# Optimization experiments

Measured on AMD Instinct MI355X. Metric: run time of the kernel, lower is better.

The kernel has to match this reference:

```python
import jax, jax.numpy as jnp
import numpy as np

N, E, G = 50000, 600000, 256
D, L, V = 128, 5, 128
BN_EPS = 1e-5


def setup_inputs() -> dict:
    key = jax.random.key(0)
    ks = jax.random.split(key, 24)
    x = jax.random.randint(ks[0], (N, 9), 0, V)
    edge_index = jax.random.randint(ks[1], (2, E), 0, N)
    edge_attr = jax.random.randint(ks[2], (E, 3), 0, V)
    batch = jnp.sort(jax.random.randint(ks[3], (N,), 0, G))
    s = 0.02
    inp = dict(
        x=x, edge_index=edge_index, edge_attr=edge_attr, batch=batch,
        atom_emb=jax.random.normal(ks[4], (9, V, D)) * s,
        bond_emb=jax.random.normal(ks[5], (L, 3, V, D)) * s,
        eps=jnp.zeros((L,)),
        W1=jax.random.normal(ks[6], (D, 2 * D)) * s, b1=jnp.zeros((2 * D,)),
        g1=jnp.ones((2 * D,)), be1=jnp.zeros((2 * D,)),
        W2=jax.random.normal(ks[7], (2 * D, D)) * s, b2=jnp.zeros((D,)),
        bn_g=jnp.ones((L, D)), bn_b=jnp.zeros((L, D)),
        fcW1=jax.random.normal(ks[8], (D, 1024)) * s, fcb1=jnp.zeros((1024,)),
        fcW2=jax.random.normal(ks[9], (1024, 1024)) * s, fcb2=jnp.zeros((1024,)),
        fcW3=jax.random.normal(ks[10], (1024, 512)) * s, fcb3=jnp.zeros((512,)),
        fcW4=jax.random.normal(ks[11], (512, 1)) * s, fcb4=jnp.zeros((1,)),
    )
    return inp


def _bn(h, g, b):
    # training-mode batchnorm (biased variance, as torch uses for normalization)
    m = h.mean(0)
    v = jnp.var(h, axis=0)
    return (h - m) * jax.lax.rsqrt(v + BN_EPS) * g + b


def _embed(tables, idx):
    # tables: [F, V, D], idx: [M, F] -> sum over F of table lookups -> [M, D]
    F = tables.shape[0]
    return tables[jnp.arange(F)[None, :], idx].sum(axis=1)


def reference(x, edge_index, edge_attr, batch, atom_emb, bond_emb, eps,
              W1, b1, g1, be1, W2, b2, bn_g, bn_b,
              fcW1, fcb1, fcW2, fcb2, fcW3, fcb3, fcW4, fcb4):
    src, dst = edge_index[0], edge_index[1]

    def mlp(h):
        z = jax.nn.relu(_bn(h @ W1 + b1, g1, be1))
        return z @ W2 + b2

    h = _embed(atom_emb, x)  # AtomEncoder: [N, D]
    h_sum = h  # JK='sum' accumulator
    for l in range(L):
        e = _embed(bond_emb[l], edge_attr)            # BondEncoder: [E, D]
        msg = jax.nn.relu(h[src] + e)                  # gather + elementwise
        agg = jax.ops.segment_sum(msg, dst, num_segments=N)  # scatter-add
        h = mlp((1.0 + eps[l]) * h + agg)
        h = _bn(h, bn_g[l], bn_b[l])
        if l < L - 1:
            h = jax.nn.relu(h)
        # dropout is identity in eval mode
        h_sum = h_sum + h

    # global mean pool over graphs
    sums = jax.ops.segment_sum(h_sum, batch, num_segments=G)
    cnts = jax.ops.segment_sum(jnp.ones((N,), h_sum.dtype), batch, num_segments=G)
    rep = sums / jnp.maximum(cnts, 1.0)[:, None]

    z = jax.nn.relu(rep @ fcW1 + fcb1)
    z = jax.nn.relu(z @ fcW2 + fcb2)
    z = jax.nn.relu(z @ fcW3 + fcb3)
    out = (z @ fcW4 + fcb4).squeeze(-1)  # [G]
    return out
```

## Files before the change

### kernel.cpp

```cpp
#include <hip/hip_runtime.h>

typedef unsigned short u16;
typedef unsigned int u32;
typedef __bf16 bf16x8 __attribute__((ext_vector_type(8)));
typedef float f32x4 __attribute__((ext_vector_type(4)));

#define NN 50000
#define EE 600000
#define GG 256
#define LL 5
#define NB 196

__device__ __forceinline__ float b2f(u16 u) {
  unsigned int v = ((unsigned int)u) << 16;
  return __builtin_bit_cast(float, v);
}
__device__ __forceinline__ u16 f2b(float f) {
  unsigned int u = __builtin_bit_cast(unsigned int, f);
  u += 0x7FFFu + ((u >> 16) & 1u);
  return (u16)(u >> 16);
}

__global__ void k_detect(const u32* __restrict__ w, int* __restrict__ flag) {
  __shared__ int sh[256];
  u32 v = w[threadIdx.x];
  u32 lo = v & 0xFFFFu;
  u32 e = (lo >> 7) & 0xFFu;
  sh[threadIdx.x] = (e >= 0x60u && e <= 0x7Fu) ? 1 : 0;
  __syncthreads();
  for (int s = 128; s > 0; s >>= 1) {
    if (threadIdx.x < (unsigned)s) sh[threadIdx.x] += sh[threadIdx.x + s];
    __syncthreads();
  }
  if (threadIdx.x == 0) flag[0] = (sh[0] < 128) ? 1 : 0;
}

struct CvtArgs {
  const void* src[19];
  u16* dst[19];
  int cum[20];
};

__global__ void k_cvt_all(CvtArgs a, const int* __restrict__ flag) {
  int t = blockIdx.x * 256 + threadIdx.x;
  if (t >= a.cum[19]) return;
  int i = 0;
  while (t >= a.cum[i + 1]) ++i;
  int j = t - a.cum[i];
  if (flag[0]) a.dst[i][j] = f2b(((const float*)a.src[i])[j]);
  else a.dst[i][j] = ((const u16*)a.src[i])[j];
}

__global__ void k_tr(const u16* __restrict__ src, u16* __restrict__ dst, int K, int N) {
  __shared__ u16 t[32][33];
  const int kb = blockIdx.x * 32, nb = blockIdx.y * 32;
  const int tx = threadIdx.x & 31, ty = threadIdx.x >> 5;
#pragma unroll
  for (int i = ty; i < 32; i += 8) t[i][tx] = src[(kb + i) * N + nb + tx];
  __syncthreads();
#pragma unroll
  for (int i = ty; i < 32; i += 8) dst[(nb + i) * K + kb + tx] = t[tx][i];
}

__global__ void k_init(int* __restrict__ deg, float* __restrict__ rep,
                       float* __restrict__ bnbuf, int* __restrict__ gstart,
                       int* __restrict__ gend) {
  int i = blockIdx.x * 256 + threadIdx.x;
  if (i < NN) deg[i] = 0;
  if (i < GG * 128) rep[i] = 0.f;
  if (i < 768) bnbuf[i] = 0.f;
  if (i < GG) { gstart[i] = 0; gend[i] = -1; }
}

__global__ void k_deg(const int* __restrict__ ei, int* __restrict__ deg) {
  int e = blockIdx.x * 256 + threadIdx.x;
  if (e < EE) atomicAdd(&deg[ei[EE + e]], 1);
}

__global__ void k_scan1(const int* __restrict__ deg, int* __restrict__ rowp,
                        int* __restrict__ bsum) {
  __shared__ int sh[256];
  int i = blockIdx.x * 256 + threadIdx.x;
  int v = (i < NN) ? deg[i] : 0;
  sh[threadIdx.x] = v;
  __syncthreads();
  for (int s = 1; s < 256; s <<= 1) {
    int t = (threadIdx.x >= (unsigned)s) ? sh[threadIdx.x - s] : 0;
    __syncthreads();
    sh[threadIdx.x] += t;
    __syncthreads();
  }
  if (i < NN) rowp[i] = sh[threadIdx.x] - v;
  if (threadIdx.x == 255) bsum[blockIdx.x] = sh[255];
}

__global__ void k_scan2(int* __restrict__ bsum, int* __restrict__ boff) {
  __shared__ int sh[256];
  int v = (threadIdx.x < NB) ? bsum[threadIdx.x] : 0;
  sh[threadIdx.x] = v;
  __syncthreads();
  for (int s = 1; s < 256; s <<= 1) {
    int t = (threadIdx.x >= (unsigned)s) ? sh[threadIdx.x - s] : 0;
    __syncthreads();
    sh[threadIdx.x] += t;
    __syncthreads();
  }
  if (threadIdx.x < NB) boff[threadIdx.x] = sh[threadIdx.x] - v;
}

__global__ void k_scan3(int* __restrict__ rowp, const int* __restrict__ boff,
                        int* __restrict__ cursor) {
  int i = blockIdx.x * 256 + threadIdx.x;
  if (i < NN) {
    int r = rowp[i] + boff[blockIdx.x];
    rowp[i] = r;
    cursor[i] = r;
  }
  if (i == 0) rowp[NN] = EE;
}

__global__ void k_fill(const int* __restrict__ ei, const int* __restrict__ eattr,
                       int* __restrict__ cursor, uint2* __restrict__ epack) {
  int e = blockIdx.x * 256 + threadIdx.x;
  if (e < EE) {
    int d = ei[EE + e];
    int pos = atomicAdd(&cursor[d], 1);
    u32 src = (u32)ei[e];
    u32 a0 = (u32)eattr[e * 3], a1 = (u32)eattr[e * 3 + 1], a2 = (u32)eattr[e * 3 + 2];
    epack[pos] = make_uint2(src | (a0 << 16) | (a1 << 23), a2);
  }
}

__global__ void k_gb(const int* __restrict__ batch, int* __restrict__ gstart,
                     int* __restrict__ gend) {
  int n = blockIdx.x * 256 + threadIdx.x;
  if (n >= NN) return;
  int b = batch[n];
  if (n == 0 || batch[n - 1] != b) gstart[b] = n;
  if (n == NN - 1 || batch[n + 1] != b) gend[b] = n;
}

__global__ void k_atom(const int* __restrict__ x, const u16* __restrict__ aemb,
                       u16* __restrict__ h) {
  int idx = blockIdx.x * 256 + threadIdx.x;
  if (idx >= NN * 64) return;
  int n = idx >> 6, f2 = (idx & 63) << 1;
  float a0 = 0.f, a1 = 0.f;
#pragma unroll
  for (int j = 0; j < 9; ++j) {
    int xv = x[n * 9 + j];
    u32 v = *(const u32*)(aemb + (j * 128 + xv) * 128 + f2);
    a0 += b2f((u16)v);
    a1 += b2f((u16)(v >> 16));
  }
  u32 o = (u32)f2b(a0) | ((u32)f2b(a1) << 16);
  *(u32*)(h + n * 128 + f2) = o;
}

__global__ __launch_bounds__(256)
void k_pull(const u16* __restrict__ h, const int* __restrict__ rowp,
            const uint2* __restrict__ epack, const u16* __restrict__ bond,
            const u16* __restrict__ epsv, int layer, u16* __restrict__ amat) {
  const int lane = threadIdx.x & 63;
  const int node = blockIdx.x * 4 + (threadIdx.x >> 6);
  const int p0 = rowp[node], p1 = rowp[node + 1];
  const int lo = lane << 1;
  const u16* bondB = bond + 16384;
  const u16* bondC = bond + 32768;
  float acc0 = 0.f, acc1 = 0.f;
  int p = p0;
  for (; p + 4 <= p1; p += 4) {
    uint2 e0 = epack[p], e1 = epack[p + 1], e2 = epack[p + 2], e3 = epack[p + 3];
    u32 h0 = *(const u32*)(h + (size_t)(e0.x & 0xFFFFu) * 128 + lo);
    u32 h1 = *(const u32*)(h + (size_t)(e1.x & 0xFFFFu) * 128 + lo);
    u32 h2 = *(const u32*)(h + (size_t)(e2.x & 0xFFFFu) * 128 + lo);
    u32 h3 = *(const u32*)(h + (size_t)(e3.x & 0xFFFFu) * 128 + lo);
    u32 a0 = *(const u32*)(bond + ((e0.x >> 16) & 0x7Fu) * 128 + lo);
    u32 a1 = *(const u32*)(bond + ((e1.x >> 16) & 0x7Fu) * 128 + lo);
    u32 a2 = *(const u32*)(bond + ((e2.x >> 16) & 0x7Fu) * 128 + lo);
    u32 a3 = *(const u32*)(bond + ((e3.x >> 16) & 0x7Fu) * 128 + lo);
    u32 b0 = *(const u32*)(bondB + ((e0.x >> 23) & 0x7Fu) * 128 + lo);
    u32 b1 = *(const u32*)(bondB + ((e1.x >> 23) & 0x7Fu) * 128 + lo);
    u32 b2 = *(const u32*)(bondB + ((e2.x >> 23) & 0x7Fu) * 128 + lo);
    u32 b3 = *(const u32*)(bondB + ((e3.x >> 23) & 0x7Fu) * 128 + lo);
    u32 c0 = *(const u32*)(bondC + e0.y * 128 + lo);
    u32 c1 = *(const u32*)(bondC + e1.y * 128 + lo);
    u32 c2 = *(const u32*)(bondC + e2.y * 128 + lo);
    u32 c3 = *(const u32*)(bondC + e3.y * 128 + lo);
    acc0 += fmaxf(b2f((u16)h0) + b2f((u16)a0) + b2f((u16)b0) + b2f((u16)c0), 0.f);
    acc1 += fmaxf(b2f((u16)(h0 >> 16)) + b2f((u16)(a0 >> 16)) + b2f((u16)(b0 >> 16)) + b2f((u16)(c0 >> 16)), 0.f);
    acc0 += fmaxf(b2f((u16)h1) + b2f((u16)a1) + b2f((u16)b1) + b2f((u16)c1), 0.f);
    acc1 += fmaxf(b2f((u16)(h1 >> 16)) + b2f((u16)(a1 >> 16)) + b2f((u16)(b1 >> 16)) + b2f((u16)(c1 >> 16)), 0.f);
    acc0 += fmaxf(b2f((u16)h2) + b2f((u16)a2) + b2f((u16)b2) + b2f((u16)c2), 0.f);
    acc1 += fmaxf(b2f((u16)(h2 >> 16)) + b2f((u16)(a2 >> 16)) + b2f((u16)(b2 >> 16)) + b2f((u16)(c2 >> 16)), 0.f);
    acc0 += fmaxf(b2f((u16)h3) + b2f((u16)a3) + b2f((u16)b3) + b2f((u16)c3), 0.f);
    acc1 += fmaxf(b2f((u16)(h3 >> 16)) + b2f((u16)(a3 >> 16)) + b2f((u16)(b3 >> 16)) + b2f((u16)(c3 >> 16)), 0.f);
  }
  for (; p < p1; ++p) {
    uint2 e0 = epack[p];
    u32 h0 = *(const u32*)(h + (size_t)(e0.x & 0xFFFFu) * 128 + lo);
    u32 a0 = *(const u32*)(bond + ((e0.x >> 16) & 0x7Fu) * 128 + lo);
    u32 b0 = *(const u32*)(bondB + ((e0.x >> 23) & 0x7Fu) * 128 + lo);
    u32 c0 = *(const u32*)(bondC + e0.y * 128 + lo);
    acc0 += fmaxf(b2f((u16)h0) + b2f((u16)a0) + b2f((u16)b0) + b2f((u16)c0), 0.f);
    acc1 += fmaxf(b2f((u16)(h0 >> 16)) + b2f((u16)(a0 >> 16)) + b2f((u16)(b0 >> 16)) + b2f((u16)(c0 >> 16)), 0.f);
  }
  float epsf = 1.0f + b2f(epsv[layer]);
  u32 own = *(const u32*)(h + (size_t)node * 128 + lo);
  u32 o = (u32)f2b(epsf * b2f((u16)own) + acc0) |
          ((u32)f2b(epsf * b2f((u16)(own >> 16)) + acc1) << 16);
  *(u32*)(amat + (size_t)node * 128 + lo) = o;
}

__global__ __launch_bounds__(256, 2)
void k_gemm1(const u16* __restrict__ amat, const u16* __restrict__ w1t,
             const u16* __restrict__ b1, u16* __restrict__ z0,
             float* __restrict__ bnsum, float* __restrict__ bnsq) {
  __shared__ u16 As[128 * 72];
  __shared__ u16 Bs[128 * 72];
  __shared__ float colAcc[256];
  const int tid = threadIdx.x;
  const int r0 = blockIdx.x * 128;
  const int nc = blockIdx.y * 128;
  const int w = tid >> 6, lane = tid & 63, l15 = lane & 15, q = lane >> 4;
  const int wr = (w & 1) * 64, wc = (w >> 1) * 64;
  f32x4 acc[4][4];
#pragma unroll
  for (int i = 0; i < 4; ++i)
#pragma unroll
    for (int j = 0; j < 4; ++j) acc[i][j] = {0.f, 0.f, 0.f, 0.f};

#pragma unroll
  for (int ks = 0; ks < 2; ++ks) {
    const int k0 = ks * 64;
    for (int idx = tid; idx < 1024; idx += 256) {
      const int row = idx >> 3, c8 = (idx & 7) << 3;
      int gr = r0 + row; if (gr >= NN) gr = NN - 1;
      uint4 va = *(const uint4*)(amat + (size_t)gr * 128 + k0 + c8);
      *(uint4*)(As + row * 72 + c8) = va;
      uint4 vb = *(const uint4*)(w1t + (size_t)(nc + row) * 128 + k0 + c8);
      *(uint4*)(Bs + row * 72 + c8) = vb;
    }
    __syncthreads();
#pragma unroll
    for (int kk = 0; kk < 64; kk += 32) {
      const int kf = kk + q * 8;
      bf16x8 a[4], b[4];
#pragma unroll
      for (int i = 0; i < 4; ++i) a[i] = *(const bf16x8*)(As + (wr + i * 16 + l15) * 72 + kf);
#pragma unroll
      for (int j = 0; j < 4; ++j) b[j] = *(const bf16x8*)(Bs + (wc + j * 16 + l15) * 72 + kf);
#pragma unroll
      for (int i = 0; i < 4; ++i)
#pragma unroll
        for (int j = 0; j < 4; ++j)
          acc[i][j] = __builtin_amdgcn_mfma_f32_16x16x32_bf16(a[i], b[j], acc[i][j], 0, 0, 0);
    }
    __syncthreads();
  }
  colAcc[tid] = 0.f;
  __syncthreads();
#pragma unroll
  for (int j = 0; j < 4; ++j) {
    const int c = wc + j * 16 + l15;
    const float bias = b2f(b1[nc + c]);
    float ls = 0.f, lsq = 0.f;
#pragma unroll
    for (int i = 0; i < 4; ++i) {
      const int gr = r0 + wr + i * 16 + q * 4;
#pragma unroll
      for (int rg = 0; rg < 4; ++rg) {
        if (gr + rg < NN) {
          const float v = acc[i][j][rg] + bias;
          z0[(gr + rg) * 256 + nc + c] = f2b(v);
          ls += v;
          lsq += v * v;
        }
      }
    }
    atomicAdd(&colAcc[c], ls);
    atomicAdd(&colAcc[128 + c], lsq);
  }
  __syncthreads();
  if (tid < 128) {
    atomicAdd(&bnsum[nc + tid], colAcc[tid]);
    atomicAdd(&bnsq[nc + tid], colAcc[128 + tid]);
  }
}

__global__ void k_bnfin(float* __restrict__ bnsum, float* __restrict__ bnsq,
                        const u16* __restrict__ g, const u16* __restrict__ b,
                        float* __restrict__ c1, float* __restrict__ c0) {
  int t = threadIdx.x;
  float s = bnsum[t], q = bnsq[t];
  bnsum[t] = 0.f;
  bnsq[t] = 0.f;
  float m = s * (1.0f / NN);
  float var = q * (1.0f / NN) - m * m;
  float rs = rsqrtf(var + 1e-5f);
  float cc1 = rs * b2f(g[t]);
  c1[t] = cc1;
  c0[t] = b2f(b[t]) - m * cc1;
}

__global__ __launch_bounds__(256, 2)
void k_gemm2(const u16* __restrict__ z0, const float* __restrict__ c1,
             const float* __restrict__ c0, const u16* __restrict__ w2t,
             const u16* __restrict__ b2, u16* __restrict__ hpre,
             float* __restrict__ bnsum, float* __restrict__ bnsq) {
  __shared__ u16 As[128 * 72];
  __shared__ u16 Bs[128 * 72];
  __shared__ float colAcc[256];
  const int tid = threadIdx.x;
  const int r0 = blockIdx.x * 128;
  const int w = tid >> 6, lane = tid & 63, l15 = lane & 15, q = lane >> 4;
  const int wr = (w & 1) * 64, wc = (w >> 1) * 64;
  f32x4 acc[4][4];
#pragma unroll
  for (int i = 0; i < 4; ++i)
#pragma unroll
    for (int j = 0; j < 4; ++j) acc[i][j] = {0.f, 0.f, 0.f, 0.f};

#pragma unroll
  for (int ks = 0; ks < 4; ++ks) {
    const int k0 = ks * 64;
    for (int idx = tid; idx < 1024; idx += 256) {
      const int row = idx >> 3, c8 = (idx & 7) << 3;
      int gr = r0 + row; if (gr >= NN) gr = NN - 1;
      ushort4 z01 = *(const ushort4*)(z0 + (size_t)gr * 256 + k0 + c8);
      ushort4 z23 = *(const ushort4*)(z0 + (size_t)gr * 256 + k0 + c8 + 4);
      ushort4 o01, o23;
      {
        const int k = k0 + c8;
        o01.x = f2b(fmaxf(b2f(z01.x) * c1[k + 0] + c0[k + 0], 0.f));
        o01.y = f2b(fmaxf(b2f(z01.y) * c1[k + 1] + c0[k + 1], 0.f));
        o01.z = f2b(fmaxf(b2f(z01.z) * c1[k + 2] + c0[k + 2], 0.f));
        o01.w = f2b(fmaxf(b2f(z01.w) * c1[k + 3] + c0[k + 3], 0.f));
        o23.x = f2b(fmaxf(b2f(z23.x) * c1[k + 4] + c0[k + 4], 0.f));
        o23.y = f2b(fmaxf(b2f(z23.y) * c1[k + 5] + c0[k + 5], 0.f));
        o23.z = f2b(fmaxf(b2f(z23.z) * c1[k + 6] + c0[k + 6], 0.f));
        o23.w = f2b(fmaxf(b2f(z23.w) * c1[k + 7] + c0[k + 7], 0.f));
      }
      *(ushort4*)(As + row * 72 + c8) = o01;
      *(ushort4*)(As + row * 72 + c8 + 4) = o23;
      uint4 vb = *(const uint4*)(w2t + (size_t)row * 256 + k0 + c8);
      *(uint4*)(Bs + row * 72 + c8) = vb;
    }
    __syncthreads();
#pragma unroll
    for (int kk = 0; kk < 64; kk += 32) {
      const int kf = kk + q * 8;
      bf16x8 a[4], b[4];
#pragma unroll
      for (int i = 0; i < 4; ++i) a[i] = *(const bf16x8*)(As + (wr + i * 16 + l15) * 72 + kf);
#pragma unroll
      for (int j = 0; j < 4; ++j) b[j] = *(const bf16x8*)(Bs + (wc + j * 16 + l15) * 72 + kf);
#pragma unroll
      for (int i = 0; i < 4; ++i)
#pragma unroll
        for (int j = 0; j < 4; ++j)
          acc[i][j] = __builtin_amdgcn_mfma_f32_16x16x32_bf16(a[i], b[j], acc[i][j], 0, 0, 0);
    }
    __syncthreads();
  }
  colAcc[tid] = 0.f;
  __syncthreads();
#pragma unroll
  for (int j = 0; j < 4; ++j) {
    const int c = wc + j * 16 + l15;
    const float bias = b2f(b2[c]);
    float ls = 0.f, lsq = 0.f;
#pragma unroll
    for (int i = 0; i < 4; ++i) {
      const int gr = r0 + wr + i * 16 + q * 4;
#pragma unroll
      for (int rg = 0; rg < 4; ++rg) {
        if (gr + rg < NN) {
          const float v = acc[i][j][rg] + bias;
          hpre[(gr + rg) * 128 + c] = f2b(v);
          ls += v;
          lsq += v * v;
        }
      }
    }
    atomicAdd(&colAcc[c], ls);
    atomicAdd(&colAcc[128 + c], lsq);
  }
  __syncthreads();
  if (tid < 128) {
    atomicAdd(&bnsum[tid], colAcc[tid]);
    atomicAdd(&bnsq[tid], colAcc[128 + tid]);
  }
}

__global__ void k_bnapply(const u16* __restrict__ hpre, const float* __restrict__ c1,
                          const float* __restrict__ c0, u16* __restrict__ h, int dorelu) {
  int idx4 = (blockIdx.x * 256 + threadIdx.x) * 4;
  if (idx4 >= NN * 128) return;
  int f = idx4 & 127;
  const ushort4 hv = *(const ushort4*)(hpre + idx4);
  const float4 rv = *(const float4*)(c1 + f);
  const float4 bv = *(const float4*)(c0 + f);
  float v0 = b2f(hv.x) * rv.x + bv.x;
  float v1 = b2f(hv.y) * rv.y + bv.y;
  float v2 = b2f(hv.z) * rv.z + bv.z;
  float v3 = b2f(hv.w) * rv.w + bv.w;
  if (dorelu) {
    v0 = fmaxf(v0, 0.f); v1 = fmaxf(v1, 0.f);
    v2 = fmaxf(v2, 0.f); v3 = fmaxf(v3, 0.f);
  }
  ushort4 ov;
  ov.x = f2b(v0); ov.y = f2b(v1); ov.z = f2b(v2); ov.w = f2b(v3);
  *(ushort4*)(h + idx4) = ov;
}

__global__ void k_poolseg(const u16* __restrict__ h, const int* __restrict__ gstart,
                          const int* __restrict__ gend, float* __restrict__ rep) {
  int g = blockIdx.x >> 2, part = blockIdx.x & 3, f = threadIdx.x;
  int r0 = gstart[g], r1 = gend[g] + 1;
  int len = r1 - r0;
  if (len <= 0) return;
  int chunk = (len + 3) >> 2;
  int s = r0 + part * chunk;
  int e = s + chunk; if (e > r1) e = r1;
  float acc = 0.f;
  for (int r = s; r < e; ++r) acc += b2f(h[r * 128 + f]);
  if (s < e) atomicAdd(&rep[g * 128 + f], acc);
}

__global__ void k_rep(float* __restrict__ rep, const int* __restrict__ gstart,
                      const int* __restrict__ gend, u16* __restrict__ repb) {
  int idx = blockIdx.x * 256 + threadIdx.x;
  int g = idx >> 7;
  int c = gend[g] - gstart[g] + 1;
  if (c < 1) c = 1;
  float v = rep[idx] / (float)c;
  rep[idx] = v;
  repb[idx] = f2b(v);
}

__global__ __launch_bounds__(256)
void k_fcg(const u16* __restrict__ A, const u16* __restrict__ Wt,
           const u16* __restrict__ bias, u16* __restrict__ out, int K, int N) {
  const int tid = threadIdx.x;
  const int r0 = blockIdx.x * 128;
  const int nc = blockIdx.y * 128;
  const int w = tid >> 6, lane = tid & 63, l15 = lane & 15, q = lane >> 4;
  const int wr = (w & 1) * 64, wc = (w >> 1) * 64;
  f32x4 acc[4][4];
#pragma unroll
  for (int i = 0; i < 4; ++i)
#pragma unroll
    for (int j = 0; j < 4; ++j) acc[i][j] = {0.f, 0.f, 0.f, 0.f};
  const int nkb = K >> 5;
  for (int kb = 0; kb < nkb; ++kb) {
    const int kf = kb * 32 + q * 8;
    bf16x8 a[4], b[4];
#pragma unroll
    for (int i = 0; i < 4; ++i)
      a[i] = *(const bf16x8*)(A + (size_t)(r0 + wr + i * 16 + l15) * K + kf);
#pragma unroll
    for (int j = 0; j < 4; ++j)
      b[j] = *(const bf16x8*)(Wt + (size_t)(nc + wc + j * 16 + l15) * K + kf);
#pragma unroll
    for (int i = 0; i < 4; ++i)
#pragma unroll
      for (int j = 0; j < 4; ++j)
        acc[i][j] = __builtin_amdgcn_mfma_f32_16x16x32_bf16(a[i], b[j], acc[i][j], 0, 0, 0);
  }
#pragma unroll
  for (int j = 0; j < 4; ++j) {
    const int c = nc + wc + j * 16 + l15;
    const float bv = b2f(bias[c]);
#pragma unroll
    for (int i = 0; i < 4; ++i) {
      const int gr = r0 + wr + i * 16 + q * 4;
#pragma unroll
      for (int rg = 0; rg < 4; ++rg)
        out[(gr + rg) * N + c] = f2b(fmaxf(acc[i][j][rg] + bv, 0.f));
    }
  }
}

__global__ void k_fc4(const u16* __restrict__ z, const u16* __restrict__ W,
                      const u16* __restrict__ bias, void* __restrict__ out,
                      const int* __restrict__ flag) {
  int g = blockIdx.x, lane = threadIdx.x;
  float acc = 0.f;
  for (int k = lane; k < 512; k += 64) acc += b2f(z[g * 512 + k]) * b2f(W[k]);
  for (int off = 32; off > 0; off >>= 1) acc += __shfl_down(acc, off);
  if (lane == 0) {
    float r = acc + b2f(bias[0]);
    if (flag[0]) ((float*)out)[g] = r;
    else ((u16*)out)[g] = f2b(r);
  }
}

extern "C" void kernel_launch(void* const* d_in, const int* in_sizes, int n_in,
                              void* d_out, int out_size, void* d_ws, size_t ws_size,
                              hipStream_t stream) {
  const int* x     = (const int*)d_in[0];
  const int* ei    = (const int*)d_in[1];
  const int* eattr = (const int*)d_in[2];
  const int* batch = (const int*)d_in[3];

  char* ws = (char*)d_ws;
  size_t off = 0;
  auto alloc = [&](size_t bytes) -> void* {
    void* p = ws + off;
    off += (bytes + 255) & ~(size_t)255;
    return p;
  };
  int* flag = (int*)alloc(256);
  u16* cvt[23];
  CvtArgs ca;
  ca.cum[0] = 0;
  for (int i = 4; i <= 22; ++i) {
    cvt[i] = (u16*)alloc((size_t)in_sizes[i] * 2);
    ca.src[i - 4] = d_in[i];
    ca.dst[i - 4] = cvt[i];
    ca.cum[i - 3] = ca.cum[i - 4] + in_sizes[i];
  }

  u16*   h      = (u16*)  alloc((size_t)NN * 128 * 2);
  u16*   amat   = (u16*)  alloc((size_t)NN * 128 * 2);
  u16*   z0     = (u16*)  alloc((size_t)NN * 256 * 2);
  u16*   w1t    = (u16*)  alloc(32768 * 2);
  u16*   w2t    = (u16*)  alloc(32768 * 2);
  u16*   ft1    = (u16*)  alloc((size_t)1024 * 128 * 2);
  u16*   ft2    = (u16*)  alloc((size_t)1024 * 1024 * 2);
  u16*   ft3    = (u16*)  alloc((size_t)512 * 1024 * 2);
  int*   deg    = (int*)  alloc((size_t)NN * 4);
  int*   cursor = (int*)  alloc((size_t)NN * 4);
  int*   rowp   = (int*)  alloc((size_t)(NN + 1) * 4);
  int*   bsum   = (int*)  alloc((size_t)NB * 4);
  int*   boff   = (int*)  alloc((size_t)NB * 4);
  uint2* epack  = (uint2*)alloc((size_t)EE * 8);
  float* bnbuf  = (float*)alloc(768 * 4);
  float* bnstat = (float*)alloc(1152 * 4);
  float* rep    = (float*)alloc((size_t)GG * 128 * 4);
  u16*   repb   = (u16*)  alloc((size_t)GG * 128 * 2);
  int*   gstart = (int*)  alloc((size_t)GG * 4);
  int*   gend   = (int*)  alloc((size_t)GG * 4);
  u16*   fz1    = (u16*)  alloc((size_t)GG * 1024 * 2);
  u16*   fz2    = (u16*)  alloc((size_t)GG * 1024 * 2);
  u16*   fz3    = (u16*)  alloc((size_t)GG * 512 * 2);
  (void)ws_size; (void)n_in; (void)out_size;

  u16* hpre = amat;

  float* bn1sum = bnbuf;
  float* bn1sq  = bnbuf + 256;
  float* bn2sum = bnbuf + 512;
  float* bn2sq  = bnbuf + 640;
  float* c1a    = bnstat;
  float* c0a    = bnstat + 256;
  float* c1b    = bnstat + 512;
  float* c0b    = bnstat + 640;

  k_detect<<<1, 256, 0, stream>>>((const u32*)d_in[4], flag);
  {
    int total = ca.cum[19];
    k_cvt_all<<<(total + 255) / 256, 256, 0, stream>>>(ca, flag);
  }
  const u16 *aembc = cvt[4], *bembc = cvt[5], *epsc = cvt[6], *w1c = cvt[7],
            *b1c = cvt[8], *g1c = cvt[9], *be1c = cvt[10], *w2c = cvt[11],
            *b2c = cvt[12], *bngc = cvt[13], *bnbc = cvt[14], *fw1 = cvt[15],
            *fb1 = cvt[16], *fw2 = cvt[17], *fb2 = cvt[18], *fw3 = cvt[19],
            *fb3 = cvt[20], *fw4 = cvt[21], *fb4 = cvt[22];

  {
    dim3 t1(4, 8), t2(8, 4), t3(4, 32), t4(32, 32), t5(32, 16);
    k_tr<<<t1, 256, 0, stream>>>(w1c, w1t, 128, 256);
    k_tr<<<t2, 256, 0, stream>>>(w2c, w2t, 256, 128);
    k_tr<<<t3, 256, 0, stream>>>(fw1, ft1, 128, 1024);
    k_tr<<<t4, 256, 0, stream>>>(fw2, ft2, 1024, 1024);
    k_tr<<<t5, 256, 0, stream>>>(fw3, ft3, 1024, 512);
  }

  k_init<<<(NN + 255) / 256, 256, 0, stream>>>(deg, rep, bnbuf, gstart, gend);
  k_deg<<<(EE + 255) / 256, 256, 0, stream>>>(ei, deg);
  k_scan1<<<NB, 256, 0, stream>>>(deg, rowp, bsum);
  k_scan2<<<1, 256, 0, stream>>>(bsum, boff);
  k_scan3<<<NB, 256, 0, stream>>>(rowp, boff, cursor);
  k_fill<<<(EE + 255) / 256, 256, 0, stream>>>(ei, eattr, cursor, epack);
  k_gb<<<(NN + 255) / 256, 256, 0, stream>>>(batch, gstart, gend);
  k_atom<<<(NN * 64 + 255) / 256, 256, 0, stream>>>(x, aembc, h);
  k_poolseg<<<GG * 4, 128, 0, stream>>>(h, gstart, gend, rep);

  const int gx = (NN + 127) / 128;
  for (int l = 0; l < LL; ++l) {
    k_pull<<<(NN + 3) / 4, 256, 0, stream>>>(h, rowp, epack,
                                             bembc + (size_t)l * 3 * 128 * 128, epsc, l, amat);
    dim3 grid1(gx, 2);
    k_gemm1<<<grid1, 256, 0, stream>>>(amat, w1t, b1c, z0, bn1sum, bn1sq);
    k_bnfin<<<1, 256, 0, stream>>>(bn1sum, bn1sq, g1c, be1c, c1a, c0a);
    k_gemm2<<<gx, 256, 0, stream>>>(z0, c1a, c0a, w2t, b2c, hpre, bn2sum, bn2sq);
    k_bnfin<<<1, 128, 0, stream>>>(bn2sum, bn2sq, bngc + l * 128, bnbc + l * 128,
                                   c1b, c0b);
    k_bnapply<<<(NN * 128) / 1024, 256, 0, stream>>>(hpre, c1b, c0b, h,
                                                     (l < LL - 1) ? 1 : 0);
    k_poolseg<<<GG * 4, 128, 0, stream>>>(h, gstart, gend, rep);
  }

  k_rep<<<(GG * 128) / 256, 256, 0, stream>>>(rep, gstart, gend, repb);
  {
    dim3 g1(2, 8), g2(2, 8), g3(2, 4);
    k_fcg<<<g1, 256, 0, stream>>>(repb, ft1, fb1, fz1, 128, 1024);
    k_fcg<<<g2, 256, 0, stream>>>(fz1, ft2, fb2, fz2, 1024, 1024);
    k_fcg<<<g3, 256, 0, stream>>>(fz2, ft3, fb3, fz3, 1024, 512);
  }
  k_fc4<<<GG, 64, 0, stream>>>(fz3, fw4, fb4, d_out, flag);
}
```

Measured before the change: 940.4 us.

## Fuse graph mean-pool accumulation into atom and bn-apply kernels via atomics

Removes the separate segment-pooling kernel and instead has each element of the atom embedding and batchnorm-apply kernels atomically add its float value into the per-graph accumulator. This drops six launches and the re-read of h for pooling. It replaces them with one global float atomic per element, which contend heavily because about 200 nodes share each graph row. The pull kernel is also rewritten to use two-wide float vectors for the bf16 unpack and accumulate, and pooling now sums unrounded fp32 values instead of bf16-rounded ones.

After: 1.472 ms. 1.57x slower.

```diff
diff --git a/kernel.cpp b/kernel.cpp
--- a/kernel.cpp
+++ b/kernel.cpp
@@ -4,6 +4,7 @@
 typedef unsigned int u32;
 typedef __bf16 bf16x8 __attribute__((ext_vector_type(8)));
 typedef float f32x4 __attribute__((ext_vector_type(4)));
+typedef float f32x2 __attribute__((ext_vector_type(2)));
 
 #define NN 50000
 #define EE 600000
@@ -19,6 +20,18 @@
   unsigned int u = __builtin_bit_cast(unsigned int, f);
   u += 0x7FFFu + ((u >> 16) & 1u);
   return (u16)(u >> 16);
+}
+__device__ __forceinline__ f32x2 up2(u32 v) {
+  f32x2 r;
+  r.x = __builtin_bit_cast(float, v << 16);
+  r.y = __builtin_bit_cast(float, v & 0xFFFF0000u);
+  return r;
+}
+__device__ __forceinline__ f32x2 max0(f32x2 v) {
+  f32x2 r;
+  r.x = fmaxf(v.x, 0.f);
+  r.y = fmaxf(v.y, 0.f);
+  return r;
 }
 
 __global__ void k_detect(const u32* __restrict__ w, int* __restrict__ flag) {
@@ -141,7 +154,8 @@
 }
 
 __global__ void k_atom(const int* __restrict__ x, const u16* __restrict__ aemb,
-                       u16* __restrict__ h) {
+                       u16* __restrict__ h, const int* __restrict__ batch,
+                       float* __restrict__ rep) {
   int idx = blockIdx.x * 256 + threadIdx.x;
   if (idx >= NN * 64) return;
   int n = idx >> 6, f2 = (idx & 63) << 1;
@@ -155,6 +169,9 @@
   }
   u32 o = (u32)f2b(a0) | ((u32)f2b(a1) << 16);
   *(u32*)(h + n * 128 + f2) = o;
+  float* r = rep + batch[n] * 128 + f2;
+  atomicAdd(r, a0);
+  atomicAdd(r + 1, a1);
 }
 
 __global__ __launch_bounds__(256)
@@ -167,7 +184,7 @@
   const int lo = lane << 1;
   const u16* bondB = bond + 16384;
   const u16* bondC = bond + 32768;
-  float acc0 = 0.f, acc1 = 0.f;
+  f32x2 acc = {0.f, 0.f};
   int p = p0;
   for (; p + 4 <= p1; p += 4) {
     uint2 e0 = epack[p], e1 = epack[p + 1], e2 = epack[p + 2], e3 = epack[p + 3];
@@ -187,14 +204,10 @@
     u32 c1 = *(const u32*)(bondC + e1.y * 128 + lo);
     u32 c2 = *(const u32*)(bondC + e2.y * 128 + lo);
     u32 c3 = *(const u32*)(bondC + e3.y * 128 + lo);
-    acc0 += fmaxf(b2f((u16)h0) + b2f((u16)a0) + b2f((u16)b0) + b2f((u16)c0), 0.f);
-    acc1 += fmaxf(b2f((u16)(h0 >> 16)) + b2f((u16)(a0 >> 16)) + b2f((u16)(b0 >> 16)) + b2f((u16)(c0 >> 16)), 0.f);
-    acc0 += fmaxf(b2f((u16)h1) + b2f((u16)a1) + b2f((u16)b1) + b2f((u16)c1), 0.f);
-    acc1 += fmaxf(b2f((u16)(h1 >> 16)) + b2f((u16)(a1 >> 16)) + b2f((u16)(b1 >> 16)) + b2f((u16)(c1 >> 16)), 0.f);
-    acc0 += fmaxf(b2f((u16)h2) + b2f((u16)a2) + b2f((u16)b2) + b2f((u16)c2), 0.f);
-    acc1 += fmaxf(b2f((u16)(h2 >> 16)) + b2f((u16)(a2 >> 16)) + b2f((u16)(b2 >> 16)) + b2f((u16)(c2 >> 16)), 0.f);
-    acc0 += fmaxf(b2f((u16)h3) + b2f((u16)a3) + b2f((u16)b3) + b2f((u16)c3), 0.f);
-    acc1 += fmaxf(b2f((u16)(h3 >> 16)) + b2f((u16)(a3 >> 16)) + b2f((u16)(b3 >> 16)) + b2f((u16)(c3 >> 16)), 0.f);
+    acc += max0(up2(h0) + up2(a0) + up2(b0) + up2(c0));
+    acc += max0(up2(h1) + up2(a1) + up2(b1) + up2(c1));
+    acc += max0(up2(h2) + up2(a2) + up2(b2) + up2(c2));
+    acc += max0(up2(h3) + up2(a3) + up2(b3) + up2(c3));
   }
   for (; p < p1; ++p) {
     uint2 e0 = epack[p];
@@ -202,13 +215,12 @@
     u32 a0 = *(const u32*)(bond + ((e0.x >> 16) & 0x7Fu) * 128 + lo);
     u32 b0 = *(const u32*)(bondB + ((e0.x >> 23) & 0x7Fu) * 128 + lo);
     u32 c0 = *(const u32*)(bondC + e0.y * 128 + lo);
-    acc0 += fmaxf(b2f((u16)h0) + b2f((u16)a0) + b2f((u16)b0) + b2f((u16)c0), 0.f);
-    acc1 += fmaxf(b2f((u16)(h0 >> 16)) + b2f((u16)(a0 >> 16)) + b2f((u16)(b0 >> 16)) + b2f((u16)(c0 >> 16)), 0.f);
+    acc += max0(up2(h0) + up2(a0) + up2(b0) + up2(c0));
   }
   float epsf = 1.0f + b2f(epsv[layer]);
   u32 own = *(const u32*)(h + (size_t)node * 128 + lo);
-  u32 o = (u32)f2b(epsf * b2f((u16)own) + acc0) |
-          ((u32)f2b(epsf * b2f((u16)(own >> 16)) + acc1) << 16);
+  f32x2 ow = up2(own);
+  u32 o = (u32)f2b(epsf * ow.x + acc.x) | ((u32)f2b(epsf * ow.y + acc.y) << 16);
   *(u32*)(amat + (size_t)node * 128 + lo) = o;
 }
 
@@ -394,10 +406,13 @@
 }
 
 __global__ void k_bnapply(const u16* __restrict__ hpre, const float* __restrict__ c1,
-                          const float* __restrict__ c0, u16* __restrict__ h, int dorelu) {
+                          const float* __restrict__ c0, u16* __restrict__ h,
+                          const int* __restrict__ batch, float* __restrict__ rep,
+                          int dorelu) {
   int idx4 = (blockIdx.x * 256 + threadIdx.x) * 4;
   if (idx4 >= NN * 128) return;
   int f = idx4 & 127;
+  int node = idx4 >> 7;
   const ushort4 hv = *(const ushort4*)(hpre + idx4);
   const float4 rv = *(const float4*)(c1 + f);
   const float4 bv = *(const float4*)(c0 + f);
@@ -412,20 +427,11 @@
   ushort4 ov;
   ov.x = f2b(v0); ov.y = f2b(v1); ov.z = f2b(v2); ov.w = f2b(v3);
   *(ushort4*)(h + idx4) = ov;
-}
-
-__global__ void k_poolseg(const u16* __restrict__ h, const int* __restrict__ gstart,
-                          const int* __restrict__ gend, float* __restrict__ rep) {
-  int g = blockIdx.x >> 2, part = blockIdx.x & 3, f = threadIdx.x;
-  int r0 = gstart[g], r1 = gend[g] + 1;
-  int len = r1 - r0;
-  if (len <= 0) return;
-  int chunk = (len + 3) >> 2;
-  int s = r0 + part * chunk;
-  int e = s + chunk; if (e > r1) e = r1;
-  float acc = 0.f;
-  for (int r = s; r < e; ++r) acc += b2f(h[r * 128 + f]);
-  if (s < e) atomicAdd(&rep[g * 128 + f], acc);
+  float* r = rep + batch[node] * 128 + f;
+  atomicAdd(r + 0, v0);
+  atomicAdd(r + 1, v1);
+  atomicAdd(r + 2, v2);
+  atomicAdd(r + 3, v3);
 }
 
 __global__ void k_rep(float* __restrict__ rep, const int* __restrict__ gstart,
@@ -537,7 +543,7 @@
   int*   boff   = (int*)  alloc((size_t)NB * 4);
   uint2* epack  = (uint2*)alloc((size_t)EE * 8);
   float* bnbuf  = (float*)alloc(768 * 4);
-  float* bnstat = (float*)alloc(1152 * 4);
+  float* bnstat = (float*)alloc(768 * 4);
   float* rep    = (float*)alloc((size_t)GG * 128 * 4);
   u16*   repb   = (u16*)  alloc((size_t)GG * 128 * 2);
   int*   gstart = (int*)  alloc((size_t)GG * 4);
@@ -585,8 +591,7 @@
   k_scan3<<<NB, 256, 0, stream>>>(rowp, boff, cursor);
   k_fill<<<(EE + 255) / 256, 256, 0, stream>>>(ei, eattr, cursor, epack);
   k_gb<<<(NN + 255) / 256, 256, 0, stream>>>(batch, gstart, gend);
-  k_atom<<<(NN * 64 + 255) / 256, 256, 0, stream>>>(x, aembc, h);
-  k_poolseg<<<GG * 4, 128, 0, stream>>>(h, gstart, gend, rep);
+  k_atom<<<(NN * 64 + 255) / 256, 256, 0, stream>>>(x, aembc, h, batch, rep);
 
   const int gx = (NN + 127) / 128;
   for (int l = 0; l < LL; ++l) {
@@ -598,9 +603,8 @@
     k_gemm2<<<gx, 256, 0, stream>>>(z0, c1a, c0a, w2t, b2c, hpre, bn2sum, bn2sq);
     k_bnfin<<<1, 128, 0, stream>>>(bn2sum, bn2sq, bngc + l * 128, bnbc + l * 128,
                                    c1b, c0b);
-    k_bnapply<<<(NN * 128) / 1024, 256, 0, stream>>>(hpre, c1b, c0b, h,
+    k_bnapply<<<(NN * 128) / 1024, 256, 0, stream>>>(hpre, c1b, c0b, h, batch, rep,
                                                      (l < LL - 1) ? 1 : 0);
-    k_poolseg<<<GG * 4, 128, 0, stream>>>(h, gstart, gend, rep);
   }
 
   k_rep<<<(GG * 128) / 256, 256, 0, stream>>>(rep, gstart, gend, repb);
```
